# Kernel optimization log

Measured on AMD Instinct MI355X. Metric: run time of the kernel, lower is better.

Reference implementation:

```python
import jax, jax.numpy as jnp
import numpy as np

B, C, H, W, HEADS = 8, 256, 64, 64, 4
EPS = 1e-5  # torch InstanceNorm2d default eps


def conv1x1(x, w):
    # w: [out_c, in_c]; x: [b, in_c, h, w]
    return jnp.einsum('oc,bchw->bohw', w, x)


def maxpool2(x):
    b, c, h, w = x.shape
    return x.reshape(b, c, h // 2, 2, w // 2, 2).max(axis=(3, 5))


def inorm_affine(x, g, b):
    # InstanceNorm2d(affine=True): normalize per (batch, channel) over H,W
    m = jnp.mean(x, axis=(2, 3), keepdims=True)
    v = jnp.mean((x - m) ** 2, axis=(2, 3), keepdims=True)
    return (x - m) * jax.lax.rsqrt(v + EPS) * g[None, :, None, None] + b[None, :, None, None]


def setup_inputs() -> dict:
    key = jax.random.key(0)
    ks = jax.random.split(key, 12)
    s = 1.0 / np.sqrt(C)  # fan-in style scaling for 1x1 conv weights
    return {
        'x': jax.random.normal(ks[0], (B, C, H, W), jnp.float32),
        'theta_w': jax.random.normal(ks[1], (C, C), jnp.float32) * s,
        'phi_w': jax.random.normal(ks[2], (C, C), jnp.float32) * s,
        'g_w': jax.random.normal(ks[3], (C // 2, C), jnp.float32) * s,
        'o_w': jax.random.normal(ks[4], (C, C // 2), jnp.float32) * np.sqrt(2.0 / C),
        'nt_w': 1.0 + 0.1 * jax.random.normal(ks[5], (C,), jnp.float32),
        'nt_b': 0.1 * jax.random.normal(ks[6], (C,), jnp.float32),
        'np_w': 1.0 + 0.1 * jax.random.normal(ks[7], (C,), jnp.float32),
        'np_b': 0.1 * jax.random.normal(ks[8], (C,), jnp.float32),
        'ng_w': 1.0 + 0.1 * jax.random.normal(ks[9], (C // 2,), jnp.float32),
        'ng_b': 0.1 * jax.random.normal(ks[10], (C // 2,), jnp.float32),
        'gamma': jnp.float32(0.5),
    }


def reference(x, theta_w, phi_w, g_w, o_w, nt_w, nt_b, np_w, np_b, ng_w, ng_b, gamma):
    b, c, h, w = x.shape
    n = h * w            # query length
    m = n // 4           # key/value length after 2x2 maxpool
    theta = inorm_affine(conv1x1(x, theta_w), nt_w, nt_b)
    phi = inorm_affine(maxpool2(conv1x1(x, phi_w)), np_w, np_b)
    g = inorm_affine(maxpool2(conv1x1(x, g_w)), ng_w, ng_b)
    # custom head layout: channel dim split as (C//heads, heads), head dim INNER
    theta_ = theta.reshape(b, c // HEADS, HEADS, n)
    phi_ = phi.reshape(b, c // HEADS, HEADS, m)
    g_ = g.reshape(b, (c // 2) // HEADS, HEADS, m)
    beta = jax.nn.softmax(jnp.einsum('bchi,bchj->bhij', theta_, phi_), axis=-1)
    o = jnp.einsum('bchj,bhij->bchi', g_, beta).reshape(b, c // 2, h, w)
    o = conv1x1(o, o_w)
    return gamma * o + x
```

## Files before the change

kernel.cpp:

```cpp
#include <hip/hip_runtime.h>
#include <hip/hip_bf16.h>
#include <math.h>

typedef float f32x4 __attribute__((ext_vector_type(4)));
typedef float f32x16 __attribute__((ext_vector_type(16)));
typedef __bf16 b16x8 __attribute__((ext_vector_type(8)));
typedef __bf16 b16x4 __attribute__((ext_vector_type(4)));
typedef unsigned int u32x2 __attribute__((ext_vector_type(2)));
typedef unsigned int u32x4 __attribute__((ext_vector_type(4)));

#define L2E 1.44269504088896340736f

__global__ void prep_weights(const float* tw, const float* pw, const float* gw,
                             const float* ow, __bf16* Wp, __bf16* OWp) {
    int idx = blockIdx.x * 256 + threadIdx.x;
    if (idx < 640 * 256) {
        int m = idx >> 8, k = idx & 255;
        float v;
        if (m < 256)      { int o = ((m & 63) << 2) + (m >> 6);            v = tw[o * 256 + k]; }
        else if (m < 512) { int mm = m - 256; int o = ((mm & 63) << 2) + (mm >> 6); v = pw[o * 256 + k]; }
        else              { int mm = m - 512; int o = ((mm & 31) << 2) + (mm >> 5); v = gw[o * 256 + k]; }
        Wp[idx] = (__bf16)v;
    } else {
        int j = idx - 640 * 256;
        if (j < 256 * 128) {
            int m = j >> 7, c = j & 127;
            int o = ((c & 31) << 2) + (c >> 5);
            OWp[j] = (__bf16)ow[m * 128 + o];
        }
    }
}

__global__ __launch_bounds__(256) void conv_gemm(const __bf16* __restrict__ Wp,
                                                 const float* __restrict__ x,
                                                 __bf16* theta_t, __bf16* phi_t, __bf16* g_t,
                                                 float* tp1, float* tp2) {
    int b = blockIdx.z, mt = blockIdx.y, nt = blockIdx.x;
    __shared__ __bf16 Al[128 * 40];
    __shared__ __bf16 Bl[128 * 40];
    int tid = threadIdx.x, l = tid & 63, w = tid >> 6;
    int wm = w >> 1, wn = w & 1, lr = l & 15, lg = l >> 4;
    f32x4 acc[4][4];
#pragma unroll
    for (int i = 0; i < 4; i++)
#pragma unroll
        for (int j = 0; j < 4; j++)
#pragma unroll
            for (int r = 0; r < 4; r++) acc[i][j][r] = 0.f;
    const __bf16* Ag = Wp + (size_t)mt * 128 * 256;
    const float* Bx = x + (size_t)b * 1048576 + nt * 128;
    int srow = tid >> 2, scol = (tid & 3) * 8;
    int bn = tid & 127, bk0 = (tid >> 7) * 8;
    b16x8 aR[2];
    float xr[2][8];
#pragma unroll
    for (int hh = 0; hh < 2; hh++)
        aR[hh] = *(const b16x8*)&Ag[(size_t)(srow + hh * 64) * 256 + scol];
#pragma unroll
    for (int u = 0; u < 2; u++)
#pragma unroll
        for (int e = 0; e < 8; e++)
            xr[u][e] = Bx[(size_t)(bk0 + u * 16 + e) * 4096 + bn];
    for (int k0 = 0; k0 < 256; k0 += 32) {
        if (k0) __syncthreads();
#pragma unroll
        for (int hh = 0; hh < 2; hh++)
            *(b16x8*)&Al[(srow + hh * 64) * 40 + scol] = aR[hh];
#pragma unroll
        for (int u = 0; u < 2; u++) {
            b16x8 v;
#pragma unroll
            for (int e = 0; e < 8; e++) v[e] = (__bf16)xr[u][e];
            *(b16x8*)&Bl[bn * 40 + bk0 + u * 16] = v;
        }
        __syncthreads();
        if (k0 < 224) {
#pragma unroll
            for (int hh = 0; hh < 2; hh++)
                aR[hh] = *(const b16x8*)&Ag[(size_t)(srow + hh * 64) * 256 + k0 + 32 + scol];
#pragma unroll
            for (int u = 0; u < 2; u++)
#pragma unroll
                for (int e = 0; e < 8; e++)
                    xr[u][e] = Bx[(size_t)(k0 + 32 + bk0 + u * 16 + e) * 4096 + bn];
        }
        int ko = lg * 8;
        b16x8 af[4], bfr[4];
#pragma unroll
        for (int i = 0; i < 4; i++) af[i]  = *(b16x8*)&Al[(wm * 64 + i * 16 + lr) * 40 + ko];
#pragma unroll
        for (int i = 0; i < 4; i++) bfr[i] = *(b16x8*)&Bl[(wn * 64 + i * 16 + lr) * 40 + ko];
#pragma unroll
        for (int i = 0; i < 4; i++)
#pragma unroll
            for (int j = 0; j < 4; j++)
                acc[i][j] = __builtin_amdgcn_mfma_f32_16x16x32_bf16(af[i], bfr[j], acc[i][j], 0, 0, 0);
    }
    if (mt < 2) {
#pragma unroll
        for (int i = 0; i < 4; i++) {
            float s1v[4], s2v[4];
#pragma unroll
            for (int r = 0; r < 4; r++) {
                float a0 = acc[i][0][r], a1 = acc[i][1][r], a2 = acc[i][2][r], a3 = acc[i][3][r];
                s1v[r] = (a0 + a1) + (a2 + a3);
                s2v[r] = (a0 * a0 + a1 * a1) + (a2 * a2 + a3 * a3);
            }
#pragma unroll
            for (int msk = 1; msk < 16; msk <<= 1)
#pragma unroll
                for (int r = 0; r < 4; r++) {
                    s1v[r] += __shfl_xor(s1v[r], msk, 64);
                    s2v[r] += __shfl_xor(s2v[r], msk, 64);
                }
            if (lr == 0) {
                int row = (b * 32 + nt) * 2 + wn;
#pragma unroll
                for (int r = 0; r < 4; r++) {
                    int ch = mt * 128 + wm * 64 + i * 16 + lg * 4 + r;
                    tp1[row * 256 + ch] = s1v[r];
                    tp2[row * 256 + ch] = s2v[r];
                }
            }
        }
    }
    int rbase = lg * 4;
#pragma unroll
    for (int i = 0; i < 4; i++) {
        int m = mt * 128 + wm * 64 + i * 16 + rbase;
#pragma unroll
        for (int j = 0; j < 4; j++) {
            int p = nt * 128 + wn * 64 + j * 16 + lr;
            b16x4 v;
#pragma unroll
            for (int r = 0; r < 4; r++) v[r] = (__bf16)acc[i][j][r];
            if (m < 256)      *(b16x4*)&theta_t[((size_t)b * 4096 + p) * 256 + m] = v;
            else if (m < 512) *(b16x4*)&phi_t[((size_t)b * 4096 + p) * 256 + (m - 256)] = v;
            else              *(b16x4*)&g_t[((size_t)b * 4096 + p) * 128 + (m - 512)] = v;
        }
    }
}

__global__ __launch_bounds__(256) void pool_phi(const __bf16* __restrict__ src, __bf16* dst,
                                                float* p1, float* p2) {
    __shared__ float S1[8][256], S2[8][256];
    int b = blockIdx.y, qc = blockIdx.x;
    int tid = threadIdx.x, cg = tid & 31, qg = tid >> 5;
    float a1[8], a2[8];
#pragma unroll
    for (int e = 0; e < 8; e++) { a1[e] = 0.f; a2[e] = 0.f; }
#pragma unroll
    for (int qq = 0; qq < 4; qq++) {
        int q = qc * 32 + qg * 4 + qq, qy = q >> 5, qx = q & 31;
        size_t base = ((size_t)(b * 4096) + qy * 128 + qx * 2) * 256 + cg * 8;
        b16x8 v0 = *(const b16x8*)&src[base];
        b16x8 v1 = *(const b16x8*)&src[base + 256];
        b16x8 v2 = *(const b16x8*)&src[base + 16384];
        b16x8 v3 = *(const b16x8*)&src[base + 16640];
        b16x8 mv;
#pragma unroll
        for (int e = 0; e < 8; e++) {
            float m = fmaxf(fmaxf((float)v0[e], (float)v1[e]), fmaxf((float)v2[e], (float)v3[e]));
            mv[e] = (__bf16)m; a1[e] += m; a2[e] += m * m;
        }
        *(b16x8*)&dst[((size_t)b * 1024 + q) * 256 + cg * 8] = mv;
    }
#pragma unroll
    for (int e = 0; e < 8; e++) { S1[qg][cg * 8 + e] = a1[e]; S2[qg][cg * 8 + e] = a2[e]; }
    __syncthreads();
    float s1 = 0.f, s2 = 0.f;
#pragma unroll
    for (int i = 0; i < 8; i++) { s1 += S1[i][tid]; s2 += S2[i][tid]; }
    p1[(b * 32 + qc) * 256 + tid] = s1;
    p2[(b * 32 + qc) * 256 + tid] = s2;
}

__global__ __launch_bounds__(256) void pool_gT(const __bf16* __restrict__ src, __bf16* gT,
                                               float* p1, float* p2) {
    __shared__ __bf16 Pt[64][136];
    __shared__ float S1[16][128], S2[16][128];
    int b = blockIdx.y, qc = blockIdx.x;
    int tid = threadIdx.x, cg = tid & 15, qg = tid >> 4;
    float a1[8], a2[8];
#pragma unroll
    for (int e = 0; e < 8; e++) { a1[e] = 0.f; a2[e] = 0.f; }
#pragma unroll
    for (int qq = 0; qq < 4; qq++) {
        int ql = qg * 4 + qq, q = qc * 64 + ql;
        int qy = q >> 5, qx = q & 31;
        size_t base = ((size_t)(b * 4096) + qy * 128 + qx * 2) * 128 + cg * 8;
        b16x8 v0 = *(const b16x8*)&src[base];
        b16x8 v1 = *(const b16x8*)&src[base + 128];
        b16x8 v2 = *(const b16x8*)&src[base + 8192];
        b16x8 v3 = *(const b16x8*)&src[base + 8320];
        b16x8 mv;
#pragma unroll
        for (int e = 0; e < 8; e++) {
            float m = fmaxf(fmaxf((float)v0[e], (float)v1[e]), fmaxf((float)v2[e], (float)v3[e]));
            mv[e] = (__bf16)m; a1[e] += m; a2[e] += m * m;
        }
        *(b16x8*)&Pt[ql][cg * 8] = mv;
    }
#pragma unroll
    for (int e = 0; e < 8; e++) { S1[qg][cg * 8 + e] = a1[e]; S2[qg][cg * 8 + e] = a2[e]; }
    __syncthreads();
    if (tid < 128) {
        float s1 = 0.f, s2 = 0.f;
#pragma unroll
        for (int i = 0; i < 16; i++) { s1 += S1[i][tid]; s2 += S2[i][tid]; }
        p1[(b * 16 + qc) * 128 + tid] = s1;
        p2[(b * 16 + qc) * 128 + tid] = s2;
    }
    int c = tid & 127, qh = tid >> 7;
    int hh = c >> 5, ch = c & 31;
#pragma unroll
    for (int sg = 0; sg < 4; sg++) {
        int seg = qh * 4 + sg;
        b16x8 v;
#pragma unroll
        for (int e = 0; e < 8; e++) v[e] = Pt[seg * 8 + e][c];
        *(b16x8*)&gT[((((size_t)(b * 4 + hh) * 16 + qc) * 8 + seg) * 32 + ch) * 8] = v;
    }
}

__global__ void finalize_stats(const float* tp1, const float* tp2, const float* pp1,
                               const float* pp2, const float* gp1, const float* gp2,
                               const float* ntw, const float* ntb, const float* npw,
                               const float* npb, const float* ngw, const float* ngb,
                               float* sct, float* bit, float* scp, float* bip,
                               float* scg, float* big) {
    int idx = blockIdx.x * 256 + threadIdx.x;
    if (idx >= 8 * 640) return;
    int b = idx / 640, c = idx % 640;
    if (c < 256) {
        float s1 = 0.f, s2 = 0.f;
        for (int i = 0; i < 64; i++) { s1 += tp1[(b * 64 + i) * 256 + c]; s2 += tp2[(b * 64 + i) * 256 + c]; }
        float n = 4096.f;
        float m = s1 / n, v = s2 / n - m * m;
        float r = rsqrtf(v + 1e-5f);
        int o = ((c & 63) << 2) + (c >> 6);
        float wv = ntw[o], bv = ntb[o];
        sct[b * 256 + c] = r * wv * L2E;
        bit[b * 256 + c] = (bv - m * r * wv) * L2E;
    } else if (c < 512) {
        int cc = c - 256;
        float s1 = 0.f, s2 = 0.f;
        for (int i = 0; i < 32; i++) { s1 += pp1[(b * 32 + i) * 256 + cc]; s2 += pp2[(b * 32 + i) * 256 + cc]; }
        float n = 1024.f;
        float m = s1 / n, v = s2 / n - m * m;
        float r = rsqrtf(v + 1e-5f);
        int o = ((cc & 63) << 2) + (cc >> 6);
        float wv = npw[o], bv = npb[o];
        scp[b * 256 + cc] = r * wv; bip[b * 256 + cc] = bv - m * r * wv;
    } else {
        int cc = c - 512;
        float s1 = 0.f, s2 = 0.f;
        for (int i = 0; i < 16; i++) { s1 += gp1[(b * 16 + i) * 128 + cc]; s2 += gp2[(b * 16 + i) * 128 + cc]; }
        float n = 1024.f;
        float m = s1 / n, v = s2 / n - m * m;
        float r = rsqrtf(v + 1e-5f);
        int o = ((cc & 31) << 2) + (cc >> 5);
        float wv = ngw[o], bv = ngb[o];
        scg[b * 128 + cc] = r * wv; big[b * 128 + cc] = bv - m * r * wv;
    }
}

__global__ void normalize_phi(const __bf16* __restrict__ php, __bf16* __restrict__ phk,
                              const float* __restrict__ scp, const float* __restrict__ bip) {
    int blk = blockIdx.x, t = threadIdx.x;
    int b = blk >> 6, h = (blk >> 4) & 3, cc = blk & 15;
#pragma unroll
    for (int uu = 0; uu < 2; uu++) {
        int u = uu * 256 + t;
        int slot = u >> 6, key = u & 63;
        int q = cc * 64 + key;
        int cfull = h * 64 + (slot >> 1) * 16 + (slot & 1) * 8;
        b16x8 v = *(const b16x8*)&php[((size_t)b * 1024 + q) * 256 + cfull];
        b16x8 nv;
#pragma unroll
        for (int e = 0; e < 8; e++)
            nv[e] = (__bf16)((float)v[e] * scp[b * 256 + cfull + e] + bip[b * 256 + cfull + e]);
        *(b16x8*)&phk[((((size_t)(b * 4 + h) * 16 + cc) * 8 + slot) * 64 + key) * 8] = nv;
    }
}

__global__ __launch_bounds__(256, 2) void attn(const __bf16* __restrict__ theta_t,
                                               const __bf16* __restrict__ phk,
                                               const __bf16* __restrict__ gTz,
                                               const float* __restrict__ sct,
                                               const float* __restrict__ bit,
                                               const float* __restrict__ scg,
                                               const float* __restrict__ big,
                                               __bf16* __restrict__ o_mid) {
    int bid = blockIdx.x;
    int idx = bid >> 3;
    int bh = (bid & 7) * 4 + (idx >> 4), qt = idx & 15;
    int b = bh >> 2, h = bh & 3;
    int tid = threadIdx.x, w = tid >> 6, lane = tid & 63;
    int l31 = lane & 31, hi = lane >> 5;
    int qb = qt * 256 + w * 64;

    b16x8 qf[2][4];
#pragma unroll
    for (int m = 0; m < 2; m++) {
        int q = qb + m * 32 + l31;
        const __bf16* qp = theta_t + ((size_t)b * 4096 + q) * 256 + h * 64;
#pragma unroll
        for (int st = 0; st < 4; st++) {
            int cb = st * 16 + hi * 8;
            b16x8 raw = *(const b16x8*)&qp[cb];
            b16x8 nv;
#pragma unroll
            for (int e = 0; e < 8; e++) {
                int cix = b * 256 + h * 64 + cb + e;
                nv[e] = (__bf16)((float)raw[e] * sct[cix] + bit[cix]);
            }
            qf[m][st] = nv;
        }
    }

    const __bf16* Kg = phk + (size_t)bh * 65536 + (size_t)hi * 512 + (size_t)l31 * 8;
    const __bf16* Vg = gTz + (size_t)bh * 32768 + (size_t)hi * 256 + (size_t)l31 * 8;

    f32x16 oacc[2];
    float l_run[2] = {0.f, 0.f};
#pragma unroll
    for (int m = 0; m < 2; m++)
#pragma unroll
        for (int r = 0; r < 16; r++) oacc[m][r] = 0.f;
    f32x16 zc;
#pragma unroll
    for (int r = 0; r < 16; r++) zc[r] = 0.f;

    b16x8 akA[2][4], avA[4], akB[2][4], avB[4];

#define LOADK(dst, c) { _Pragma("unroll") for (int kf = 0; kf < 2; kf++) \
    _Pragma("unroll") for (int st = 0; st < 4; st++) \
        dst[kf][st] = *(const b16x8*)&Kg[(size_t)(c) * 4096 + st * 1024 + kf * 256]; }
#define LOADV(dst, c) { _Pragma("unroll") for (int js = 0; js < 4; js++) \
    dst[js] = *(const b16x8*)&Vg[(size_t)(c) * 2048 + js * 512]; }
#define COMPUTE(ak, av) { \
    _Pragma("unroll") for (int m = 0; m < 2; m++) { \
        _Pragma("unroll") for (int kf = 0; kf < 2; kf++) { \
            f32x16 s = __builtin_amdgcn_mfma_f32_32x32x16_bf16(ak[kf][0], qf[m][0], zc, 0, 0, 0); \
            _Pragma("unroll") for (int st = 1; st < 4; st++) \
                s = __builtin_amdgcn_mfma_f32_32x32x16_bf16(ak[kf][st], qf[m][st], s, 0, 0, 0); \
            float sum = 0.f; \
            _Pragma("unroll") for (int r = 0; r < 16; r++) { \
                float p = __builtin_amdgcn_exp2f(s[r]); s[r] = p; sum += p; } \
            l_run[m] += sum; \
            _Pragma("unroll") for (int hh2 = 0; hh2 < 2; hh2++) { \
                b16x4 A4, B4; \
                _Pragma("unroll") for (int e = 0; e < 4; e++) { \
                    A4[e] = (__bf16)s[hh2 * 8 + e]; B4[e] = (__bf16)s[hh2 * 8 + 4 + e]; } \
                u32x2 a2 = __builtin_bit_cast(u32x2, A4); \
                u32x2 b2 = __builtin_bit_cast(u32x2, B4); \
                u32x2 q0 = __builtin_amdgcn_permlane32_swap(a2[0], b2[0], false, false); \
                u32x2 q1 = __builtin_amdgcn_permlane32_swap(a2[1], b2[1], false, false); \
                u32x4 pd = {q0[0], q1[0], q0[1], q1[1]}; \
                b16x8 pf = __builtin_bit_cast(b16x8, pd); \
                oacc[m] = __builtin_amdgcn_mfma_f32_32x32x16_bf16(av[kf * 2 + hh2], pf, oacc[m], 0, 0, 0); \
            } \
        } \
    } }

    LOADK(akA, 0) LOADV(avA, 0)
#pragma unroll 1
    for (int c = 0; c < 16; c += 2) {
        LOADK(akB, c + 1) LOADV(avB, c + 1)
        COMPUTE(akA, avA)
        if (c + 2 < 16) { LOADK(akA, c + 2) LOADV(avA, c + 2) }
        COMPUTE(akB, avB)
    }
#undef LOADK
#undef LOADV
#undef COMPUTE

#pragma unroll
    for (int m = 0; m < 2; m++) {
        float lr = l_run[m] + __shfl_xor(l_run[m], 32, 64);
        float rl = 1.0f / lr;
        int q = qb + m * 32 + l31;
#pragma unroll
        for (int rr = 0; rr < 4; rr++) {
            b16x4 v;
#pragma unroll
            for (int e = 0; e < 4; e++) {
                int ci = b * 128 + h * 32 + rr * 8 + hi * 4 + e;
                v[e] = (__bf16)(oacc[m][rr * 4 + e] * rl * scg[ci] + big[ci]);
            }
            *(b16x4*)&o_mid[((size_t)b * 4096 + q) * 128 + h * 32 + rr * 8 + hi * 4] = v;
        }
    }
}

__global__ __launch_bounds__(256) void out_gemm(const __bf16* __restrict__ OWp,
                                                const __bf16* __restrict__ o_mid,
                                                const float* __restrict__ x,
                                                const float* gamma, float* out) {
    int b = blockIdx.z, mt = blockIdx.y, nt = blockIdx.x;
    __shared__ __bf16 Al[128 * 40];
    __shared__ __bf16 Bl[128 * 40];
    int tid = threadIdx.x, l = tid & 63, w = tid >> 6;
    int wm = w >> 1, wn = w & 1, lr = l & 15, lg = l >> 4;
    f32x4 acc[4][4];
#pragma unroll
    for (int i = 0; i < 4; i++)
#pragma unroll
        for (int j = 0; j < 4; j++)
#pragma unroll
            for (int r = 0; r < 4; r++) acc[i][j][r] = 0.f;
    const __bf16* Ag = OWp + (size_t)mt * 128 * 128;
    const __bf16* Bg = o_mid + ((size_t)b * 4096 + nt * 128) * 128;
    int srow = tid >> 2, scol = (tid & 3) * 8;
    b16x8 aR[2], bR[2];
#pragma unroll
    for (int hh = 0; hh < 2; hh++) {
        int r = srow + hh * 64;
        aR[hh] = *(const b16x8*)&Ag[(size_t)r * 128 + scol];
        bR[hh] = *(const b16x8*)&Bg[(size_t)r * 128 + scol];
    }
    for (int k0 = 0; k0 < 128; k0 += 32) {
        if (k0) __syncthreads();
#pragma unroll
        for (int hh = 0; hh < 2; hh++) {
            int r = srow + hh * 64;
            *(b16x8*)&Al[r * 40 + scol] = aR[hh];
            *(b16x8*)&Bl[r * 40 + scol] = bR[hh];
        }
        __syncthreads();
        if (k0 < 96) {
#pragma unroll
            for (int hh = 0; hh < 2; hh++) {
                int r = srow + hh * 64;
                aR[hh] = *(const b16x8*)&Ag[(size_t)r * 128 + k0 + 32 + scol];
                bR[hh] = *(const b16x8*)&Bg[(size_t)r * 128 + k0 + 32 + scol];
            }
        }
        int ko = lg * 8;
        b16x8 af[4], bfr[4];
#pragma unroll
        for (int i = 0; i < 4; i++) af[i]  = *(b16x8*)&Al[(wm * 64 + i * 16 + lr) * 40 + ko];
#pragma unroll
        for (int i = 0; i < 4; i++) bfr[i] = *(b16x8*)&Bl[(wn * 64 + i * 16 + lr) * 40 + ko];
#pragma unroll
        for (int i = 0; i < 4; i++)
#pragma unroll
            for (int j = 0; j < 4; j++)
                acc[i][j] = __builtin_amdgcn_mfma_f32_16x16x32_bf16(af[i], bfr[j], acc[i][j], 0, 0, 0);
    }
    float gm = gamma[0];
    int rbase = lg * 4;
#pragma unroll
    for (int i = 0; i < 4; i++) {
        int m = mt * 128 + wm * 64 + i * 16 + rbase;
#pragma unroll
        for (int j = 0; j < 4; j++) {
            int p = nt * 128 + wn * 64 + j * 16 + lr;
#pragma unroll
            for (int r = 0; r < 4; r++) {
                size_t o = ((size_t)b * 256 + m + r) * 4096 + p;
                __builtin_nontemporal_store(gm * acc[i][j][r] + x[o], &out[o]);
            }
        }
    }
}

extern "C" void kernel_launch(void* const* d_in, const int* in_sizes, int n_in,
                              void* d_out, int out_size, void* d_ws, size_t ws_size,
                              hipStream_t stream) {
    const float* x   = (const float*)d_in[0];
    const float* tw  = (const float*)d_in[1];
    const float* pw  = (const float*)d_in[2];
    const float* gw  = (const float*)d_in[3];
    const float* ow  = (const float*)d_in[4];
    const float* ntw = (const float*)d_in[5];
    const float* ntb = (const float*)d_in[6];
    const float* npw = (const float*)d_in[7];
    const float* npb = (const float*)d_in[8];
    const float* ngw = (const float*)d_in[9];
    const float* ngb = (const float*)d_in[10];
    const float* gamma = (const float*)d_in[11];
    float* out = (float*)d_out;
    char* ws = (char*)d_ws;

    __bf16* Wp  = (__bf16*)(ws + 0);
    __bf16* OWp = (__bf16*)(ws + 327680);
    __bf16* th  = (__bf16*)(ws + 17170432);
    __bf16* phr = (__bf16*)(ws + 33947648);
    __bf16* ghr = (__bf16*)(ws + 50724864);
    __bf16* php = (__bf16*)(ws + 59113472);
    __bf16* gT  = (__bf16*)(ws + 63307776);
    float* sb   = (float*)(ws + 65445888);

    float* tp1 = (float*)(ws + 393216);
    float* tp2 = (float*)(ws + 917504);
    float* pp1 = (float*)(ws + 1441792);
    float* pp2 = (float*)(ws + 1703936);
    float* gp1 = (float*)(ws + 1966080);
    float* gp2 = (float*)(ws + 2031616);
    __bf16* phk = phr;
    __bf16* om  = (__bf16*)(ws + 2097152);

    float *sct = sb, *bit = sb + 2048, *scp = sb + 4096, *bip = sb + 6144,
          *scg = sb + 8192, *big = sb + 9216;

    prep_weights<<<768, 256, 0, stream>>>(tw, pw, gw, ow, Wp, OWp);
    conv_gemm<<<dim3(32, 5, 8), 256, 0, stream>>>(Wp, x, th, phr, ghr, tp1, tp2);
    pool_phi<<<dim3(32, 8), 256, 0, stream>>>(phr, php, pp1, pp2);
    pool_gT<<<dim3(16, 8), 256, 0, stream>>>(ghr, gT, gp1, gp2);
    finalize_stats<<<20, 256, 0, stream>>>(tp1, tp2, pp1, pp2, gp1, gp2,
                                           ntw, ntb, npw, npb, ngw, ngb,
                                           sct, bit, scp, bip, scg, big);
    normalize_phi<<<512, 256, 0, stream>>>(php, phk, scp, bip);
    attn<<<512, 256, 0, stream>>>(th, phk, gT, sct, bit, scg, big, om);
    out_gemm<<<dim3(32, 2, 8), 256, 0, stream>>>(OWp, om, x, gamma, out);
}
```

Baseline: 115.7 us.

## Fuse maxpool and stat partials into conv GEMM epilogue, fold phi norm into query

Phi and g maxpooling, per-channel partial statistics and the key/value relayout move into the conv GEMM epilogue through shared memory. This removes the pool_phi, pool_gT and normalize_phi kernels and the full-resolution phi/g intermediate buffers. The phi instance-norm affine is folded algebraically into the query: the query is scaled by the phi scale, and a per-query bias dot product is added before the exponent. This saves memory traffic and launches, but the epilogue gets heavier, and the folded bias rounds differently in bf16.

Result: faster. 107.0 us (median of 2 runs) (-7.5%).

```diff
diff --git a/kernel.cpp b/kernel.cpp
--- a/kernel.cpp
+++ b/kernel.cpp
@@ -33,11 +33,17 @@
 
 __global__ __launch_bounds__(256) void conv_gemm(const __bf16* __restrict__ Wp,
                                                  const float* __restrict__ x,
-                                                 __bf16* theta_t, __bf16* phi_t, __bf16* g_t,
-                                                 float* tp1, float* tp2) {
+                                                 __bf16* theta_t, __bf16* phk, __bf16* gT,
+                                                 float* tp1, float* tp2,
+                                                 float* pp1, float* pp2,
+                                                 float* gp1, float* gp2) {
+    __shared__ __align__(16) char smem[38912];
+    __bf16* Al = (__bf16*)smem;
+    __bf16* Bl = (__bf16*)(smem + 10240);
+    __bf16* Pl = (__bf16*)smem;
+    float* S1w = (float*)(smem + 34816);
+    float* S2w = (float*)(smem + 36864);
     int b = blockIdx.z, mt = blockIdx.y, nt = blockIdx.x;
-    __shared__ __bf16 Al[128 * 40];
-    __shared__ __bf16 Bl[128 * 40];
     int tid = threadIdx.x, l = tid & 63, w = tid >> 6;
     int wm = w >> 1, wn = w & 1, lr = l & 15, lg = l >> 4;
     f32x4 acc[4][4];
@@ -123,103 +129,106 @@
                 }
             }
         }
-    }
-    int rbase = lg * 4;
-#pragma unroll
-    for (int i = 0; i < 4; i++) {
-        int m = mt * 128 + wm * 64 + i * 16 + rbase;
-#pragma unroll
-        for (int j = 0; j < 4; j++) {
-            int p = nt * 128 + wn * 64 + j * 16 + lr;
-            b16x4 v;
-#pragma unroll
-            for (int r = 0; r < 4; r++) v[r] = (__bf16)acc[i][j][r];
-            if (m < 256)      *(b16x4*)&theta_t[((size_t)b * 4096 + p) * 256 + m] = v;
-            else if (m < 512) *(b16x4*)&phi_t[((size_t)b * 4096 + p) * 256 + (m - 256)] = v;
-            else              *(b16x4*)&g_t[((size_t)b * 4096 + p) * 128 + (m - 512)] = v;
-        }
-    }
-}
-
-__global__ __launch_bounds__(256) void pool_phi(const __bf16* __restrict__ src, __bf16* dst,
-                                                float* p1, float* p2) {
-    __shared__ float S1[8][256], S2[8][256];
-    int b = blockIdx.y, qc = blockIdx.x;
-    int tid = threadIdx.x, cg = tid & 31, qg = tid >> 5;
-    float a1[8], a2[8];
-#pragma unroll
-    for (int e = 0; e < 8; e++) { a1[e] = 0.f; a2[e] = 0.f; }
-#pragma unroll
-    for (int qq = 0; qq < 4; qq++) {
-        int q = qc * 32 + qg * 4 + qq, qy = q >> 5, qx = q & 31;
-        size_t base = ((size_t)(b * 4096) + qy * 128 + qx * 2) * 256 + cg * 8;
-        b16x8 v0 = *(const b16x8*)&src[base];
-        b16x8 v1 = *(const b16x8*)&src[base + 256];
-        b16x8 v2 = *(const b16x8*)&src[base + 16384];
-        b16x8 v3 = *(const b16x8*)&src[base + 16640];
-        b16x8 mv;
+        int rbase = lg * 4;
+#pragma unroll
+        for (int i = 0; i < 4; i++) {
+            int m = mt * 128 + wm * 64 + i * 16 + rbase;
+#pragma unroll
+            for (int j = 0; j < 4; j++) {
+                int p = nt * 128 + wn * 64 + j * 16 + lr;
+                b16x4 v;
+#pragma unroll
+                for (int r = 0; r < 4; r++) v[r] = (__bf16)acc[i][j][r];
+                *(b16x4*)&theta_t[((size_t)b * 4096 + p) * 256 + m] = v;
+            }
+        }
+    } else {
+        __syncthreads();
+        int rbase = lg * 4;
+#pragma unroll
+        for (int i = 0; i < 4; i++) {
+            int ch = wm * 64 + i * 16 + rbase;
+#pragma unroll
+            for (int j = 0; j < 4; j++) {
+                int p = wn * 64 + j * 16 + lr;
+                b16x4 v;
+#pragma unroll
+                for (int r = 0; r < 4; r++) v[r] = (__bf16)acc[i][j][r];
+                *(b16x4*)&Pl[p * 136 + ch] = v;
+            }
+        }
+        __syncthreads();
+        int o = tid & 15, tq = tid >> 4;
+        float a1[8], a2[8];
+#pragma unroll
+        for (int e = 0; e < 8; e++) { a1[e] = 0.f; a2[e] = 0.f; }
+        b16x8 pooled[2];
+#pragma unroll
+        for (int ss = 0; ss < 2; ss++) {
+            int xq = tq * 2 + ss;
+            b16x8 v0 = *(b16x8*)&Pl[(2 * xq) * 136 + o * 8];
+            b16x8 v1 = *(b16x8*)&Pl[(2 * xq + 1) * 136 + o * 8];
+            b16x8 v2 = *(b16x8*)&Pl[(64 + 2 * xq) * 136 + o * 8];
+            b16x8 v3 = *(b16x8*)&Pl[(65 + 2 * xq) * 136 + o * 8];
+            b16x8 mv;
+#pragma unroll
+            for (int e = 0; e < 8; e++) {
+                float m = fmaxf(fmaxf((float)v0[e], (float)v1[e]), fmaxf((float)v2[e], (float)v3[e]));
+                mv[e] = (__bf16)m; a1[e] += m; a2[e] += m * m;
+            }
+            pooled[ss] = mv;
+        }
 #pragma unroll
         for (int e = 0; e < 8; e++) {
-            float m = fmaxf(fmaxf((float)v0[e], (float)v1[e]), fmaxf((float)v2[e], (float)v3[e]));
-            mv[e] = (__bf16)m; a1[e] += m; a2[e] += m * m;
-        }
-        *(b16x8*)&dst[((size_t)b * 1024 + q) * 256 + cg * 8] = mv;
-    }
-#pragma unroll
-    for (int e = 0; e < 8; e++) { S1[qg][cg * 8 + e] = a1[e]; S2[qg][cg * 8 + e] = a2[e]; }
-    __syncthreads();
-    float s1 = 0.f, s2 = 0.f;
-#pragma unroll
-    for (int i = 0; i < 8; i++) { s1 += S1[i][tid]; s2 += S2[i][tid]; }
-    p1[(b * 32 + qc) * 256 + tid] = s1;
-    p2[(b * 32 + qc) * 256 + tid] = s2;
-}
-
-__global__ __launch_bounds__(256) void pool_gT(const __bf16* __restrict__ src, __bf16* gT,
-                                               float* p1, float* p2) {
-    __shared__ __bf16 Pt[64][136];
-    __shared__ float S1[16][128], S2[16][128];
-    int b = blockIdx.y, qc = blockIdx.x;
-    int tid = threadIdx.x, cg = tid & 15, qg = tid >> 4;
-    float a1[8], a2[8];
-#pragma unroll
-    for (int e = 0; e < 8; e++) { a1[e] = 0.f; a2[e] = 0.f; }
-#pragma unroll
-    for (int qq = 0; qq < 4; qq++) {
-        int ql = qg * 4 + qq, q = qc * 64 + ql;
-        int qy = q >> 5, qx = q & 31;
-        size_t base = ((size_t)(b * 4096) + qy * 128 + qx * 2) * 128 + cg * 8;
-        b16x8 v0 = *(const b16x8*)&src[base];
-        b16x8 v1 = *(const b16x8*)&src[base + 128];
-        b16x8 v2 = *(const b16x8*)&src[base + 8192];
-        b16x8 v3 = *(const b16x8*)&src[base + 8320];
-        b16x8 mv;
-#pragma unroll
-        for (int e = 0; e < 8; e++) {
-            float m = fmaxf(fmaxf((float)v0[e], (float)v1[e]), fmaxf((float)v2[e], (float)v3[e]));
-            mv[e] = (__bf16)m; a1[e] += m; a2[e] += m * m;
-        }
-        *(b16x8*)&Pt[ql][cg * 8] = mv;
-    }
-#pragma unroll
-    for (int e = 0; e < 8; e++) { S1[qg][cg * 8 + e] = a1[e]; S2[qg][cg * 8 + e] = a2[e]; }
-    __syncthreads();
-    if (tid < 128) {
-        float s1 = 0.f, s2 = 0.f;
-#pragma unroll
-        for (int i = 0; i < 16; i++) { s1 += S1[i][tid]; s2 += S2[i][tid]; }
-        p1[(b * 16 + qc) * 128 + tid] = s1;
-        p2[(b * 16 + qc) * 128 + tid] = s2;
-    }
-    int c = tid & 127, qh = tid >> 7;
-    int hh = c >> 5, ch = c & 31;
-#pragma unroll
-    for (int sg = 0; sg < 4; sg++) {
-        int seg = qh * 4 + sg;
-        b16x8 v;
-#pragma unroll
-        for (int e = 0; e < 8; e++) v[e] = Pt[seg * 8 + e][c];
-        *(b16x8*)&gT[((((size_t)(b * 4 + hh) * 16 + qc) * 8 + seg) * 32 + ch) * 8] = v;
+            a1[e] += __shfl_xor(a1[e], 16, 64); a1[e] += __shfl_xor(a1[e], 32, 64);
+            a2[e] += __shfl_xor(a2[e], 16, 64); a2[e] += __shfl_xor(a2[e], 32, 64);
+        }
+        if ((tid & 63) < 16) {
+#pragma unroll
+            for (int e = 0; e < 8; e++) {
+                S1w[w * 128 + o * 8 + e] = a1[e];
+                S2w[w * 128 + o * 8 + e] = a2[e];
+            }
+        }
+        __syncthreads();
+        int cc = nt >> 1;
+        if (mt < 4) {
+            if (tid < 128) {
+                float s1 = S1w[tid] + S1w[128 + tid] + S1w[256 + tid] + S1w[384 + tid];
+                float s2 = S2w[tid] + S2w[128 + tid] + S2w[256 + tid] + S2w[384 + tid];
+                pp1[(size_t)(b * 32 + nt) * 256 + (mt - 2) * 128 + tid] = s1;
+                pp2[(size_t)(b * 32 + nt) * 256 + (mt - 2) * 128 + tid] = s2;
+            }
+            int hh = (mt - 2) * 2 + (o >> 3), slot = o & 7, bh = b * 4 + hh;
+#pragma unroll
+            for (int ss = 0; ss < 2; ss++) {
+                int key = (nt & 1) * 32 + tq * 2 + ss;
+                *(b16x8*)&phk[((((size_t)bh * 16 + cc) * 8 + slot) * 64 + key) * 8] = pooled[ss];
+            }
+        } else {
+            if (tid < 128) {
+                float s1 = S1w[tid] + S1w[128 + tid] + S1w[256 + tid] + S1w[384 + tid];
+                float s2 = S2w[tid] + S2w[128 + tid] + S2w[256 + tid] + S2w[384 + tid];
+                gp1[(size_t)(b * 32 + nt) * 128 + tid] = s1;
+                gp2[(size_t)(b * 32 + nt) * 128 + tid] = s2;
+            }
+            __bf16* Pg = Pl;
+#pragma unroll
+            for (int ss = 0; ss < 2; ss++)
+                *(b16x8*)&Pg[(tq * 2 + ss) * 136 + o * 8] = pooled[ss];
+            __syncthreads();
+            int ch = tid & 127, kg = tid >> 7;
+            int hh = ch >> 5, c32 = ch & 31, bh = b * 4 + hh;
+#pragma unroll
+            for (int gi = 0; gi < 2; gi++) {
+                int g2 = kg * 2 + gi;
+                b16x8 v;
+#pragma unroll
+                for (int e = 0; e < 8; e++) v[e] = Pg[(g2 * 8 + e) * 136 + ch];
+                int seg = (nt & 1) * 4 + g2;
+                *(b16x8*)&gT[((((size_t)bh * 16 + cc) * 8 + seg) * 32 + c32) * 8] = v;
+            }
+        }
     }
 }
 
@@ -255,7 +264,7 @@
     } else {
         int cc = c - 512;
         float s1 = 0.f, s2 = 0.f;
-        for (int i = 0; i < 16; i++) { s1 += gp1[(b * 16 + i) * 128 + cc]; s2 += gp2[(b * 16 + i) * 128 + cc]; }
+        for (int i = 0; i < 32; i++) { s1 += gp1[(b * 32 + i) * 128 + cc]; s2 += gp2[(b * 32 + i) * 128 + cc]; }
         float n = 1024.f;
         float m = s1 / n, v = s2 / n - m * m;
         float r = rsqrtf(v + 1e-5f);
@@ -265,30 +274,13 @@
     }
 }
 
-__global__ void normalize_phi(const __bf16* __restrict__ php, __bf16* __restrict__ phk,
-                              const float* __restrict__ scp, const float* __restrict__ bip) {
-    int blk = blockIdx.x, t = threadIdx.x;
-    int b = blk >> 6, h = (blk >> 4) & 3, cc = blk & 15;
-#pragma unroll
-    for (int uu = 0; uu < 2; uu++) {
-        int u = uu * 256 + t;
-        int slot = u >> 6, key = u & 63;
-        int q = cc * 64 + key;
-        int cfull = h * 64 + (slot >> 1) * 16 + (slot & 1) * 8;
-        b16x8 v = *(const b16x8*)&php[((size_t)b * 1024 + q) * 256 + cfull];
-        b16x8 nv;
-#pragma unroll
-        for (int e = 0; e < 8; e++)
-            nv[e] = (__bf16)((float)v[e] * scp[b * 256 + cfull + e] + bip[b * 256 + cfull + e]);
-        *(b16x8*)&phk[((((size_t)(b * 4 + h) * 16 + cc) * 8 + slot) * 64 + key) * 8] = nv;
-    }
-}
-
 __global__ __launch_bounds__(256, 2) void attn(const __bf16* __restrict__ theta_t,
                                                const __bf16* __restrict__ phk,
                                                const __bf16* __restrict__ gTz,
                                                const float* __restrict__ sct,
                                                const float* __restrict__ bit,
+                                               const float* __restrict__ scp,
+                                               const float* __restrict__ bip,
                                                const float* __restrict__ scg,
                                                const float* __restrict__ big,
                                                __bf16* __restrict__ o_mid) {
@@ -301,8 +293,10 @@
     int qb = qt * 256 + w * 64;
 
     b16x8 qf[2][4];
+    float cq[2];
 #pragma unroll
     for (int m = 0; m < 2; m++) {
+        cq[m] = 0.f;
         int q = qb + m * 32 + l31;
         const __bf16* qp = theta_t + ((size_t)b * 4096 + q) * 256 + h * 64;
 #pragma unroll
@@ -313,10 +307,13 @@
 #pragma unroll
             for (int e = 0; e < 8; e++) {
                 int cix = b * 256 + h * 64 + cb + e;
-                nv[e] = (__bf16)((float)raw[e] * sct[cix] + bit[cix]);
+                float thn = (float)raw[e] * sct[cix] + bit[cix];
+                cq[m] += thn * bip[cix];
+                nv[e] = (__bf16)(thn * scp[cix]);
             }
             qf[m][st] = nv;
         }
+        cq[m] += __shfl_xor(cq[m], 32, 64);
     }
 
     const __bf16* Kg = phk + (size_t)bh * 65536 + (size_t)hi * 512 + (size_t)l31 * 8;
@@ -341,13 +338,14 @@
     dst[js] = *(const b16x8*)&Vg[(size_t)(c) * 2048 + js * 512]; }
 #define COMPUTE(ak, av) { \
     _Pragma("unroll") for (int m = 0; m < 2; m++) { \
+        float cqm = cq[m]; \
         _Pragma("unroll") for (int kf = 0; kf < 2; kf++) { \
             f32x16 s = __builtin_amdgcn_mfma_f32_32x32x16_bf16(ak[kf][0], qf[m][0], zc, 0, 0, 0); \
             _Pragma("unroll") for (int st = 1; st < 4; st++) \
                 s = __builtin_amdgcn_mfma_f32_32x32x16_bf16(ak[kf][st], qf[m][st], s, 0, 0, 0); \
             float sum = 0.f; \
             _Pragma("unroll") for (int r = 0; r < 16; r++) { \
-                float p = __builtin_amdgcn_exp2f(s[r]); s[r] = p; sum += p; } \
+                float p = __builtin_amdgcn_exp2f(s[r] + cqm); s[r] = p; sum += p; } \
             l_run[m] += sum; \
             _Pragma("unroll") for (int hh2 = 0; hh2 < 2; hh2++) { \
                 b16x4 A4, B4; \
@@ -486,33 +484,27 @@
 
     __bf16* Wp  = (__bf16*)(ws + 0);
     __bf16* OWp = (__bf16*)(ws + 327680);
-    __bf16* th  = (__bf16*)(ws + 17170432);
-    __bf16* phr = (__bf16*)(ws + 33947648);
-    __bf16* ghr = (__bf16*)(ws + 50724864);
-    __bf16* php = (__bf16*)(ws + 59113472);
-    __bf16* gT  = (__bf16*)(ws + 63307776);
-    float* sb   = (float*)(ws + 65445888);
-
-    float* tp1 = (float*)(ws + 393216);
-    float* tp2 = (float*)(ws + 917504);
-    float* pp1 = (float*)(ws + 1441792);
-    float* pp2 = (float*)(ws + 1703936);
-    float* gp1 = (float*)(ws + 1966080);
-    float* gp2 = (float*)(ws + 2031616);
-    __bf16* phk = phr;
-    __bf16* om  = (__bf16*)(ws + 2097152);
+    float* tp1  = (float*)(ws + 393216);
+    float* tp2  = (float*)(ws + 917504);
+    float* pp1  = (float*)(ws + 1441792);
+    float* pp2  = (float*)(ws + 1703936);
+    float* gp1  = (float*)(ws + 1966080);
+    float* gp2  = (float*)(ws + 2097152);
+    float* sb   = (float*)(ws + 2228224);
+    __bf16* th  = (__bf16*)(ws + 2269184);
+    __bf16* phk = (__bf16*)(ws + 19046400);
+    __bf16* gT  = (__bf16*)(ws + 23240704);
+    __bf16* om  = (__bf16*)(ws + 25337856);
 
     float *sct = sb, *bit = sb + 2048, *scp = sb + 4096, *bip = sb + 6144,
           *scg = sb + 8192, *big = sb + 9216;
 
     prep_weights<<<768, 256, 0, stream>>>(tw, pw, gw, ow, Wp, OWp);
-    conv_gemm<<<dim3(32, 5, 8), 256, 0, stream>>>(Wp, x, th, phr, ghr, tp1, tp2);
-    pool_phi<<<dim3(32, 8), 256, 0, stream>>>(phr, php, pp1, pp2);
-    pool_gT<<<dim3(16, 8), 256, 0, stream>>>(ghr, gT, gp1, gp2);
+    conv_gemm<<<dim3(32, 5, 8), 256, 0, stream>>>(Wp, x, th, phk, gT,
+                                                  tp1, tp2, pp1, pp2, gp1, gp2);
     finalize_stats<<<20, 256, 0, stream>>>(tp1, tp2, pp1, pp2, gp1, gp2,
                                            ntw, ntb, npw, npb, ngw, ngb,
                                            sct, bit, scp, bip, scg, big);
-    normalize_phi<<<512, 256, 0, stream>>>(php, phk, scp, bip);
-    attn<<<512, 256, 0, stream>>>(th, phk, gT, sct, bit, scg, big, om);
+    attn<<<512, 256, 0, stream>>>(th, phk, gT, sct, bit, scp, bip, scg, big, om);
     out_gemm<<<dim3(32, 2, 8), 256, 0, stream>>>(OWp, om, x, gamma, out);
 }
```
